# Kernel tuning notes

Hardware: AMD Instinct MI355X
Metric: run time of the kernel (lower is better)

## Reference

```python
import jax, jax.numpy as jnp
import numpy as np

B, D, H = 65536, 3, 256  # collocation batch, coord dim, hidden width


def setup_inputs() -> dict:
    key = jax.random.key(0)
    ks = jax.random.split(key, 8)

    def init(k, shape, fan_in):
        return jax.random.normal(k, shape, dtype=jnp.float32) * np.float32(1.0 / np.sqrt(fan_in))

    return {
        "x": jax.random.uniform(ks[0], (B, D), dtype=jnp.float32, minval=0.1, maxval=1.0),
        "W0": init(ks[1], (D, H), D), "b0": jnp.zeros((H,), jnp.float32),
        "W1": init(ks[2], (H, H), H), "b1": jnp.zeros((H,), jnp.float32),
        "W2": init(ks[3], (H, H), H), "b2": jnp.zeros((H,), jnp.float32),
        "W3": init(ks[4], (H, H), H), "b3": jnp.zeros((H,), jnp.float32),
        "Wout": init(ks[5], (H, 1), H), "bout": jnp.zeros((1,), jnp.float32),
    }


def reference(x, W0, b0, W1, b1, W2, b2, W3, b3, Wout, bout):
    # Scalar PINN network u(xi), xi: [D]
    def u_fn(xi):
        h = jnp.tanh(xi @ W0 + b0)
        h = jnp.tanh(h @ W1 + b1)
        h = jnp.tanh(h @ W2 + b2)
        h = jnp.tanh(h @ W3 + b3)
        return (h @ Wout + bout)[0]

    u = jax.vmap(u_fn)(x)                               # [B]
    # batch_gradient: du/dx_i for every coordinate axis (Cartesian: no adjustment)
    grads = jax.vmap(jax.grad(u_fn))(x)                 # [B, D]
    # batch_hessian diagonal: d^2u/dx_i^2 via forward-over-reverse
    hess_fn = jax.jacfwd(jax.grad(u_fn))                # [D, D] per sample
    hess_diag = jax.vmap(lambda xi: jnp.diagonal(hess_fn(xi)))(x)  # [B, D]
    # pack (u, grad, hessian-diagonal) as the PDE-residual ingredients
    return jnp.concatenate([u[:, None], grads, hess_diag], axis=1)  # [B, 1+D+D]
```

## Files before the change

### kernel.cpp

```cpp
#include <hip/hip_runtime.h>
#include <hip/hip_fp16.h>

#define HDIM 256
#define MS 16
#define LDAK 264
#define CSTRIDE (MS * LDAK * 2)

typedef _Float16 half8 __attribute__((ext_vector_type(8)));
typedef _Float16 half4 __attribute__((ext_vector_type(4)));
typedef _Float16 half2v __attribute__((ext_vector_type(2)));
typedef float f32x4 __attribute__((ext_vector_type(4)));

__device__ __forceinline__ float fast_tanh(float x) {
    float e = __expf(2.0f * x);
    return 1.0f - 2.0f * __builtin_amdgcn_rcpf(e + 1.0f);
}

__device__ __forceinline__ half4 cvt4(float a, float b, float c, float d) {
    half2v lo = __builtin_bit_cast(half2v, __builtin_amdgcn_cvt_pkrtz(a, b));
    half2v hi = __builtin_bit_cast(half2v, __builtin_amdgcn_cvt_pkrtz(c, d));
    half4 r; r[0] = lo[0]; r[1] = lo[1]; r[2] = hi[0]; r[3] = hi[1];
    return r;
}

__device__ __forceinline__ void barrier_lds() {
    asm volatile("s_waitcnt lgkmcnt(0)\n\ts_barrier" ::: "memory");
}

__global__ __launch_bounds__(256) void pack_weights(const float* __restrict__ W1,
                                                    const float* __restrict__ W2,
                                                    const float* __restrict__ W3,
                                                    _Float16* __restrict__ out) {
    int tid = blockIdx.x * 256 + threadIdx.x;
    int l = tid >> 13;
    int idx = tid & 8191;
    int kg = idx >> 8;
    int n = idx & 255;
    const float* W = (l == 0) ? W1 : (l == 1) ? W2 : W3;
    half8 v;
    #pragma unroll
    for (int j = 0; j < 8; ++j) v[j] = (_Float16)W[(kg * 8 + j) * 256 + n];
    *(half8*)(out + l * 65536 + kg * 2048 + n * 8) = v;
}

__global__ __launch_bounds__(256, 2)
void pinn_fused(const float* __restrict__ x,
                const float* __restrict__ W0,
                const float* __restrict__ b0,
                const float* __restrict__ b1,
                const float* __restrict__ b2,
                const float* __restrict__ b3,
                const float* __restrict__ Wout,
                const float* __restrict__ bout,
                const _Float16* __restrict__ Wp,
                float* __restrict__ out) {
    __shared__ __align__(16) _Float16 Abuf[7 * MS][LDAK];
    __shared__ float part[4 * 7 * MS];

    const int tid  = threadIdx.x;
    const int lane = tid & 63;
    const int wid  = tid >> 6;
    const int qd   = lane >> 4;
    const int n15  = lane & 15;
    const int base = blockIdx.x * MS;
    const int nw   = wid * 64 + n15;

    const _Float16* Wbase = Wp + (qd * 256 + nw) * 8;

    const char* Ab = (const char*)Abuf;
    const int abase = (n15 * LDAK + qd * 8) * 2;
    char* Sb = (char*)Abuf;
    const int sbase = (n15 * LDAK + wid * 64 + qd * 4) * 2;

    half8 wf[2][4];

#define PREF(G) do { \
    if ((G) < 24) { \
        _Pragma("unroll") \
        for (int t_ = 0; t_ < 4; ++t_) \
            wf[(G) & 1][t_] = *(const half8*)(Wbase + (G) * 8192 + t_ * 128); \
    } \
} while (0)

#define LDAF(AF, S) do { \
    _Pragma("unroll") \
    for (int c_ = 0; c_ < 7; ++c_) \
        AF[c_] = *(const half8*)(Ab + abase + c_ * CSTRIDE + (S) * 64); \
} while (0)

#define MMS(ACC, AF, G) do { \
    PREF((G) + 1); \
    __builtin_amdgcn_s_setprio(1); \
    _Pragma("unroll") \
    for (int c_ = 0; c_ < 7; ++c_) \
        _Pragma("unroll") \
        for (int t_ = 0; t_ < 4; ++t_) \
            ACC[c_][t_] = __builtin_amdgcn_mfma_f32_16x16x32_f16(wf[(G) & 1][t_], AF[c_], ACC[c_][t_], 0, 0, 0); \
    __builtin_amdgcn_s_setprio(0); \
} while (0)

#define KLOOP(ACC, G0) do { \
    half8 afX[7], afY[7]; \
    LDAF(afX, 0); \
    LDAF(afY, 1); \
    MMS(ACC, afX, (G0) + 0); \
    LDAF(afX, 2); \
    MMS(ACC, afY, (G0) + 1); \
    LDAF(afY, 3); \
    MMS(ACC, afX, (G0) + 2); \
    LDAF(afX, 4); \
    MMS(ACC, afY, (G0) + 3); \
    LDAF(afY, 5); \
    MMS(ACC, afX, (G0) + 4); \
    LDAF(afX, 6); \
    MMS(ACC, afY, (G0) + 5); \
    LDAF(afY, 7); \
    MMS(ACC, afX, (G0) + 6); \
    MMS(ACC, afY, (G0) + 7); \
} while (0)

#define ZACC(A_) do { \
    _Pragma("unroll") \
    for (int c_ = 0; c_ < 7; ++c_) \
        _Pragma("unroll") \
        for (int t_ = 0; t_ < 4; ++t_) A_[c_][t_] = (f32x4){0.f, 0.f, 0.f, 0.f}; \
} while (0)

    PREF(0);

    {
        const int m  = tid & 15;
        const int nb = (tid >> 4) * 16;
        const float x0 = x[(base + m) * 3 + 0];
        const float x1 = x[(base + m) * 3 + 1];
        const float x2 = x[(base + m) * 3 + 2];
        #pragma unroll
        for (int ch = 0; ch < 2; ++ch) {
            const int n0 = nb + ch * 8;
            f32x4 w0v[2], w1v[2], w2v[2], bv[2];
            w0v[0] = *(const f32x4*)(W0 + n0);            w0v[1] = *(const f32x4*)(W0 + n0 + 4);
            w1v[0] = *(const f32x4*)(W0 + HDIM + n0);     w1v[1] = *(const f32x4*)(W0 + HDIM + n0 + 4);
            w2v[0] = *(const f32x4*)(W0 + 2 * HDIM + n0); w2v[1] = *(const f32x4*)(W0 + 2 * HDIM + n0 + 4);
            bv[0]  = *(const f32x4*)(b0 + n0);            bv[1]  = *(const f32x4*)(b0 + n0 + 4);
            half8 h[7];
            #pragma unroll
            for (int r = 0; r < 8; ++r) {
                const float w0 = w0v[r >> 2][r & 3];
                const float w1 = w1v[r >> 2][r & 3];
                const float w2 = w2v[r >> 2][r & 3];
                float z  = x0 * w0 + x1 * w1 + x2 * w2 + bv[r >> 2][r & 3];
                float tv = fast_tanh(z);
                float dd = 1.f - tv * tv;
                float c2 = -2.f * tv * dd;
                h[0][r] = (_Float16)tv;
                h[1][r] = (_Float16)(dd * w0);
                h[2][r] = (_Float16)(dd * w1);
                h[3][r] = (_Float16)(dd * w2);
                h[4][r] = (_Float16)(c2 * w0 * w0);
                h[5][r] = (_Float16)(c2 * w1 * w1);
                h[6][r] = (_Float16)(c2 * w2 * w2);
            }
            #pragma unroll
            for (int c = 0; c < 7; ++c)
                *(half8*)&Abuf[c * MS + m][n0] = h[c];
        }
    }
    barrier_lds();

    #pragma unroll
    for (int l = 0; l < 2; ++l) {
        const float* bb = (l == 0) ? b1 : b2;

        f32x4 acc[7][4];
        ZACC(acc);
        KLOOP(acc, l * 8);
        barrier_lds();

        #pragma unroll
        for (int t = 0; t < 4; ++t) {
            const int ncol = wid * 64 + t * 16 + qd * 4;
            f32x4 bv = *(const f32x4*)(bb + ncol);
            float tv[4], gj[3][4], sj[3][4];
            #pragma unroll
            for (int r = 0; r < 4; ++r) {
                float zv = acc[0][t][r] + bv[r];
                tv[r] = fast_tanh(zv);
                float dd = 1.f - tv[r] * tv[r];
                float c2 = -2.f * tv[r] * dd;
                #pragma unroll
                for (int i = 0; i < 3; ++i) {
                    float zg = acc[1 + i][t][r];
                    float zs = acc[4 + i][t][r];
                    gj[i][r] = dd * zg;
                    sj[i][r] = dd * zs + c2 * zg * zg;
                }
            }
            *(half4*)(Sb + sbase + 0 * CSTRIDE + t * 32) = cvt4(tv[0], tv[1], tv[2], tv[3]);
            #pragma unroll
            for (int i = 0; i < 3; ++i) {
                *(half4*)(Sb + sbase + (1 + i) * CSTRIDE + t * 32) =
                    cvt4(gj[i][0], gj[i][1], gj[i][2], gj[i][3]);
                *(half4*)(Sb + sbase + (4 + i) * CSTRIDE + t * 32) =
                    cvt4(sj[i][0], sj[i][1], sj[i][2], sj[i][3]);
            }
        }
        barrier_lds();
    }

    {
        f32x4 acc[7][4];
        ZACC(acc);
        KLOOP(acc, 16);

        float p[7] = {0.f, 0.f, 0.f, 0.f, 0.f, 0.f, 0.f};
        #pragma unroll
        for (int t = 0; t < 4; ++t) {
            const int ncol = wid * 64 + t * 16 + qd * 4;
            f32x4 bv = *(const f32x4*)(b3 + ncol);
            f32x4 wv = *(const f32x4*)(Wout + ncol);
            #pragma unroll
            for (int r = 0; r < 4; ++r) {
                float zv = acc[0][t][r] + bv[r];
                float tv = fast_tanh(zv);
                float dd = 1.f - tv * tv;
                float c2 = -2.f * tv * dd;
                p[0] += tv * wv[r];
                #pragma unroll
                for (int i = 0; i < 3; ++i) {
                    float zg = acc[1 + i][t][r];
                    float zs = acc[4 + i][t][r];
                    p[1 + i] += (dd * zg) * wv[r];
                    p[4 + i] += (dd * zs + c2 * zg * zg) * wv[r];
                }
            }
        }
        #pragma unroll
        for (int c = 0; c < 7; ++c) {
            p[c] += __shfl_xor(p[c], 16, 64);
            p[c] += __shfl_xor(p[c], 32, 64);
        }
        if (lane < 16) {
            #pragma unroll
            for (int c = 0; c < 7; ++c)
                part[(wid * 7 + c) * MS + lane] = p[c];
        }
    }
    barrier_lds();

    if (tid < 7 * MS) {
        const int c = tid >> 4;
        const int m = tid & 15;
        float v = part[(0 * 7 + c) * MS + m] + part[(1 * 7 + c) * MS + m] +
                  part[(2 * 7 + c) * MS + m] + part[(3 * 7 + c) * MS + m];
        if (c == 0) v += bout[0];
        out[(base + m) * 7 + c] = v;
    }

#undef PREF
#undef LDAF
#undef MMS
#undef KLOOP
#undef ZACC
}

extern "C" void kernel_launch(void* const* d_in, const int* in_sizes, int n_in,
                              void* d_out, int out_size, void* d_ws, size_t ws_size,
                              hipStream_t stream) {
    const float* xp   = (const float*)d_in[0];
    const float* W0   = (const float*)d_in[1];
    const float* b0   = (const float*)d_in[2];
    const float* W1   = (const float*)d_in[3];
    const float* b1   = (const float*)d_in[4];
    const float* W2   = (const float*)d_in[5];
    const float* b2   = (const float*)d_in[6];
    const float* W3   = (const float*)d_in[7];
    const float* b3   = (const float*)d_in[8];
    const float* Wout = (const float*)d_in[9];
    const float* bout = (const float*)d_in[10];
    _Float16* Wp = (_Float16*)d_ws;

    pack_weights<<<96, 256, 0, stream>>>(W1, W2, W3, Wp);
    pinn_fused<<<65536 / MS, 256, 0, stream>>>(xp, W0, b0, b1, b2, b3, Wout, bout, Wp,
                                               (float*)d_out);
}
```

Measured before the change: 242.3 us.

## Rotate per-wave K order so each wave starts on self-produced slices before barrier

Each wave now walks the K dimension in a rotated order that starts with the two 32-column slices it wrote itself. Those two slices are multiplied before the LDS barrier, and the rest after it, so MFMA work overlaps the barrier wait. The elementwise tanh/derivative epilogue is computed into registers before the barrier and stored to LDS after it, which lets the next layer start early. This relies on the wave-to-column ownership mapping staying consistent. It also raises register pressure by holding a half4[7][4] staging array.

```diff
diff --git a/kernel.cpp b/kernel.cpp
--- a/kernel.cpp
+++ b/kernel.cpp
@@ -64,6 +64,7 @@
     const int n15  = lane & 15;
     const int base = blockIdx.x * MS;
     const int nw   = wid * 64 + n15;
+    const int rot  = wid * 2;
 
     const _Float16* Wbase = Wp + (qd * 256 + nw) * 8;
 
@@ -74,49 +75,49 @@
 
     half8 wf[2][4];
 
-#define PREF(G) do { \
-    if ((G) < 24) { \
+#define PREFJ(JJ) do { \
+    if ((JJ) < 24) { \
+        const int g_ = (((JJ) >> 3) * 8 + ((rot + ((JJ) & 7)) & 7)); \
         _Pragma("unroll") \
         for (int t_ = 0; t_ < 4; ++t_) \
-            wf[(G) & 1][t_] = *(const half8*)(Wbase + (G) * 8192 + t_ * 128); \
+            wf[(JJ) & 1][t_] = *(const half8*)(Wbase + g_ * 8192 + t_ * 128); \
     } \
 } while (0)
 
-#define LDAF(AF, S) do { \
+#define LDAFS(AF, I) do { \
+    const int so_ = ((rot + (I)) & 7) * 64; \
     _Pragma("unroll") \
     for (int c_ = 0; c_ < 7; ++c_) \
-        AF[c_] = *(const half8*)(Ab + abase + c_ * CSTRIDE + (S) * 64); \
-} while (0)
-
-#define MMS(ACC, AF, G) do { \
-    PREF((G) + 1); \
+        AF[c_] = *(const half8*)(Ab + abase + c_ * CSTRIDE + so_); \
+} while (0)
+
+#define MMSJ(ACC, AF, JJ) do { \
+    PREFJ((JJ) + 1); \
     __builtin_amdgcn_s_setprio(1); \
     _Pragma("unroll") \
     for (int c_ = 0; c_ < 7; ++c_) \
         _Pragma("unroll") \
         for (int t_ = 0; t_ < 4; ++t_) \
-            ACC[c_][t_] = __builtin_amdgcn_mfma_f32_16x16x32_f16(wf[(G) & 1][t_], AF[c_], ACC[c_][t_], 0, 0, 0); \
+            ACC[c_][t_] = __builtin_amdgcn_mfma_f32_16x16x32_f16(wf[(JJ) & 1][t_], AF[c_], ACC[c_][t_], 0, 0, 0); \
     __builtin_amdgcn_s_setprio(0); \
 } while (0)
 
-#define KLOOP(ACC, G0) do { \
+#define KPRE(ACC, L) do { \
     half8 afX[7], afY[7]; \
-    LDAF(afX, 0); \
-    LDAF(afY, 1); \
-    MMS(ACC, afX, (G0) + 0); \
-    LDAF(afX, 2); \
-    MMS(ACC, afY, (G0) + 1); \
-    LDAF(afY, 3); \
-    MMS(ACC, afX, (G0) + 2); \
-    LDAF(afX, 4); \
-    MMS(ACC, afY, (G0) + 3); \
-    LDAF(afY, 5); \
-    MMS(ACC, afX, (G0) + 4); \
-    LDAF(afX, 6); \
-    MMS(ACC, afY, (G0) + 5); \
-    LDAF(afY, 7); \
-    MMS(ACC, afX, (G0) + 6); \
-    MMS(ACC, afY, (G0) + 7); \
+    LDAFS(afX, 0); LDAFS(afY, 1); \
+    MMSJ(ACC, afX, (L) * 8 + 0); \
+    MMSJ(ACC, afY, (L) * 8 + 1); \
+} while (0)
+
+#define KPOST(ACC, L) do { \
+    half8 afX[7], afY[7]; \
+    LDAFS(afX, 2); LDAFS(afY, 3); \
+    MMSJ(ACC, afX, (L) * 8 + 2); LDAFS(afX, 4); \
+    MMSJ(ACC, afY, (L) * 8 + 3); LDAFS(afY, 5); \
+    MMSJ(ACC, afX, (L) * 8 + 4); LDAFS(afX, 6); \
+    MMSJ(ACC, afY, (L) * 8 + 5); LDAFS(afY, 7); \
+    MMSJ(ACC, afX, (L) * 8 + 6); \
+    MMSJ(ACC, afY, (L) * 8 + 7); \
 } while (0)
 
 #define ZACC(A_) do { \
@@ -126,7 +127,48 @@
         for (int t_ = 0; t_ < 4; ++t_) A_[c_][t_] = (f32x4){0.f, 0.f, 0.f, 0.f}; \
 } while (0)
 
-    PREF(0);
+#define ELEMC(ACC, BB, EV) do { \
+    _Pragma("unroll") \
+    for (int tt_ = 0; tt_ < 4; ++tt_) { \
+        const int ncol_ = wid * 64 + tt_ * 16 + qd * 4; \
+        f32x4 bv_ = *(const f32x4*)((BB) + ncol_); \
+        float tv_[4], gj_[3][4], sj_[3][4]; \
+        _Pragma("unroll") \
+        for (int r_ = 0; r_ < 4; ++r_) { \
+            float zv_ = ACC[0][tt_][r_] + bv_[r_]; \
+            tv_[r_] = fast_tanh(zv_); \
+            float dd_ = 1.f - tv_[r_] * tv_[r_]; \
+            float c2_ = -2.f * tv_[r_] * dd_; \
+            _Pragma("unroll") \
+            for (int i_ = 0; i_ < 3; ++i_) { \
+                float zg_ = ACC[1 + i_][tt_][r_]; \
+                float zs_ = ACC[4 + i_][tt_][r_]; \
+                gj_[i_][r_] = dd_ * zg_; \
+                sj_[i_][r_] = dd_ * zs_ + c2_ * zg_ * zg_; \
+            } \
+        } \
+        EV[0][tt_] = cvt4(tv_[0], tv_[1], tv_[2], tv_[3]); \
+        _Pragma("unroll") \
+        for (int i_ = 0; i_ < 3; ++i_) { \
+            EV[1 + i_][tt_] = cvt4(gj_[i_][0], gj_[i_][1], gj_[i_][2], gj_[i_][3]); \
+            EV[4 + i_][tt_] = cvt4(sj_[i_][0], sj_[i_][1], sj_[i_][2], sj_[i_][3]); \
+        } \
+    } \
+} while (0)
+
+#define ELEMS(EV) do { \
+    _Pragma("unroll") \
+    for (int c_ = 0; c_ < 7; ++c_) \
+        _Pragma("unroll") \
+        for (int tt_ = 0; tt_ < 4; ++tt_) \
+            *(half4*)(Sb + sbase + c_ * CSTRIDE + tt_ * 32) = EV[c_][tt_]; \
+} while (0)
+
+    f32x4 acc[7][4];
+    half4 ev[7][4];
+
+    ZACC(acc);
+    PREFJ(0);
 
     {
         const int m  = tid & 15;
@@ -165,53 +207,27 @@
                 *(half8*)&Abuf[c * MS + m][n0] = h[c];
         }
     }
-    barrier_lds();
-
-    #pragma unroll
-    for (int l = 0; l < 2; ++l) {
-        const float* bb = (l == 0) ? b1 : b2;
-
-        f32x4 acc[7][4];
-        ZACC(acc);
-        KLOOP(acc, l * 8);
-        barrier_lds();
-
-        #pragma unroll
-        for (int t = 0; t < 4; ++t) {
-            const int ncol = wid * 64 + t * 16 + qd * 4;
-            f32x4 bv = *(const f32x4*)(bb + ncol);
-            float tv[4], gj[3][4], sj[3][4];
-            #pragma unroll
-            for (int r = 0; r < 4; ++r) {
-                float zv = acc[0][t][r] + bv[r];
-                tv[r] = fast_tanh(zv);
-                float dd = 1.f - tv[r] * tv[r];
-                float c2 = -2.f * tv[r] * dd;
-                #pragma unroll
-                for (int i = 0; i < 3; ++i) {
-                    float zg = acc[1 + i][t][r];
-                    float zs = acc[4 + i][t][r];
-                    gj[i][r] = dd * zg;
-                    sj[i][r] = dd * zs + c2 * zg * zg;
-                }
-            }
-            *(half4*)(Sb + sbase + 0 * CSTRIDE + t * 32) = cvt4(tv[0], tv[1], tv[2], tv[3]);
-            #pragma unroll
-            for (int i = 0; i < 3; ++i) {
-                *(half4*)(Sb + sbase + (1 + i) * CSTRIDE + t * 32) =
-                    cvt4(gj[i][0], gj[i][1], gj[i][2], gj[i][3]);
-                *(half4*)(Sb + sbase + (4 + i) * CSTRIDE + t * 32) =
-                    cvt4(sj[i][0], sj[i][1], sj[i][2], sj[i][3]);
-            }
-        }
-        barrier_lds();
-    }
-
+    KPRE(acc, 0);
+    barrier_lds();
+
+    KPOST(acc, 0);
+    ELEMC(acc, b1, ev);
+    barrier_lds();
+    ELEMS(ev);
+    ZACC(acc);
+    KPRE(acc, 1);
+    barrier_lds();
+
+    KPOST(acc, 1);
+    ELEMC(acc, b2, ev);
+    barrier_lds();
+    ELEMS(ev);
+    ZACC(acc);
+    KPRE(acc, 2);
+    barrier_lds();
+
+    KPOST(acc, 2);
     {
-        f32x4 acc[7][4];
-        ZACC(acc);
-        KLOOP(acc, 16);
-
         float p[7] = {0.f, 0.f, 0.f, 0.f, 0.f, 0.f, 0.f};
         #pragma unroll
         for (int t = 0; t < 4; ++t) {
@@ -256,11 +272,14 @@
         out[(base + m) * 7 + c] = v;
     }
 
-#undef PREF
-#undef LDAF
-#undef MMS
-#undef KLOOP
+#undef PREFJ
+#undef LDAFS
+#undef MMSJ
+#undef KPRE
+#undef KPOST
 #undef ZACC
+#undef ELEMC
+#undef ELEMS
 }
 
 extern "C" void kernel_launch(void* const* d_in, const int* in_sizes, int n_in,
```

After: 246.6 us (median of 2 runs). Within noise of the previous version (+1.8%).
